# Performance work log

Hardware: AMD Instinct MI355X
Metric: run time of the kernel (lower is better)

## Reference

```python
import jax, jax.numpy as jnp
import numpy as np

V_A, V_HP = 256, 256
H_A, H_HP = 2048, 4096
DEPTH = 12


def lstm_cell(x, h, c, W_ih, W_hh, b_ih, b_hh):
    # PyTorch LSTM cell: gate order i, f, g, o along the 4H axis.
    gates = x @ W_ih.T + h @ W_hh.T + (b_ih + b_hh)
    i, f, g, o = jnp.split(gates, 4, axis=-1)
    c_new = jax.nn.sigmoid(f) * c + jax.nn.sigmoid(i) * jnp.tanh(g)
    h_new = jax.nn.sigmoid(o) * jnp.tanh(c_new)
    return h_new, c_new


def setup_inputs() -> dict:
    key = jax.random.key(0)
    ks = jax.random.split(key, 16)
    s = jnp.float32(0.02)
    f32 = jnp.float32
    return {
        "x_thought_vec_arch": jax.random.normal(ks[0], (1, 1, H_A), f32),
        "x_thought_vec_arch_hp": jax.random.normal(ks[1], (1, 1, H_HP), f32),
        # arch LSTM (input V_A, hidden H_A)
        "W_ih_a": jax.random.normal(ks[2], (4 * H_A, V_A), f32) * s,
        "W_hh_a": jax.random.normal(ks[3], (4 * H_A, H_A), f32) * s,
        "b_ih_a": jax.random.normal(ks[4], (4 * H_A,), f32) * s,
        "b_hh_a": jax.random.normal(ks[5], (4 * H_A,), f32) * s,
        # arch_out Linear (H_A -> V_A)
        "W_out_a": jax.random.normal(ks[6], (V_A, H_A), f32) * s,
        "b_out_a": jax.random.normal(ks[7], (V_A,), f32) * s,
        # hp_summarizer Linear (H_HP -> H_HP//2)
        "W_sum": jax.random.normal(ks[8], (H_HP // 2, H_HP), f32) * s,
        "b_sum": jax.random.normal(ks[9], (H_HP // 2,), f32) * s,
        # arch_hp LSTM (input V_A + V_HP, hidden H_HP)
        "W_ih_hp": jax.random.normal(ks[10], (4 * H_HP, V_A + V_HP), f32) * s,
        "W_hh_hp": jax.random.normal(ks[11], (4 * H_HP, H_HP), f32) * s,
        "b_ih_hp": jax.random.normal(ks[12], (4 * H_HP,), f32) * s,
        "b_hh_hp": jax.random.normal(ks[13], (4 * H_HP,), f32) * s,
        # arch_hp_out Linear (H_HP -> V_HP)
        "W_out_hp": jax.random.normal(ks[14], (V_HP, H_HP), f32) * s,
        "b_out_hp": jax.random.normal(ks[15], (V_HP,), f32) * s,
    }


def reference(x_thought_vec_arch, x_thought_vec_arch_hp,
              W_ih_a, W_hh_a, b_ih_a, b_hh_a, W_out_a, b_out_a,
              W_sum, b_sum, W_ih_hp, W_hh_hp, b_ih_hp, b_hh_hp,
              W_out_hp, b_out_hp):
    h_a, h_hp = x_thought_vec_arch, x_thought_vec_arch_hp  # thought vecs used as hidden states
    c_a = jnp.zeros_like(h_a)
    c_hp = jnp.zeros_like(h_hp)
    a = jnp.full((1, 1, V_A), 1.0 / V_A, jnp.float32)       # SOS soft one-hot
    a_hp = jnp.full((1, 1, V_HP), 1.0 / V_HP, jnp.float32)

    def step(carry, _):
        a, a_hp, h_a, c_a, h_hp, c_hp = carry
        # forward_arch: seq_len=1 so LSTM output == new hidden
        h_a, c_a = lstm_cell(a, h_a, c_a, W_ih_a, W_hh_a, b_ih_a, b_hh_a)
        a = jax.nn.softmax(h_a @ W_out_a.T + b_out_a, axis=-1)
        # forward_arch_hp (keeps the original's swapped hx=(c_hp, prev_h_hp)):
        h_sum = jax.nn.relu(h_hp @ W_sum.T + b_sum)
        prev_h_hp = jnp.concatenate([h_a, h_sum], axis=-1)   # used as CELL state
        inp = jnp.concatenate([a, a_hp], axis=-1)
        h_hp, c_hp = lstm_cell(inp, c_hp, prev_h_hp, W_ih_hp, W_hh_hp, b_ih_hp, b_hh_hp)
        a_hp = jax.nn.softmax(h_hp @ W_out_hp.T + b_out_hp, axis=-1)
        return (a, a_hp, h_a, c_a, h_hp, c_hp), (a, a_hp)

    _, (ys_a, ys_hp) = jax.lax.scan(step, (a, a_hp, h_a, c_a, h_hp, c_hp), None, length=DEPTH)
    # torch.cat(list_of_(1,1,V), dim=1) -> (1, DEPTH, V)
    arch = ys_a.reshape(DEPTH, V_A)[None]
    arch_hp = ys_hp.reshape(DEPTH, V_HP)[None]
    return arch, arch_hp
```

## Files before the change

### kernel.cpp

```cpp
#include <hip/hip_runtime.h>
#include <hip/hip_fp16.h>

#define H_A   2048
#define H_HP  4096
#define DEPTH 12

struct Half8 { __half2 a, b, c, d; };
struct Half4 { __half2 a, b; };

__device__ __forceinline__ float fsig_(float x) { return 1.0f / (1.0f + __expf(-x)); }
__device__ __forceinline__ float ftanh_(float x) {
    return 1.0f - 2.0f / (__expf(2.0f * x) + 1.0f);
}
__device__ __forceinline__ float dot4_(float4 a, float4 b) {
    return a.x * b.x + a.y * b.y + a.z * b.z + a.w * b.w;
}
__device__ __forceinline__ float dot8h_(Half8 w, float4 x0, float4 x1) {
    float2 wa = __half22float2(w.a), wb = __half22float2(w.b);
    float2 wc = __half22float2(w.c), wd = __half22float2(w.d);
    return wa.x * x0.x + wa.y * x0.y + wb.x * x0.z + wb.y * x0.w +
           wc.x * x1.x + wc.y * x1.y + wd.x * x1.z + wd.y * x1.w;
}
__device__ __forceinline__ Half4 cvt4_(float4 a) {
    Half4 h;
    h.a = __floats2half2_rn(a.x, a.y);
    h.b = __floats2half2_rn(a.z, a.w);
    return h;
}
__device__ __forceinline__ Half8 cvt8_(float4 a, float4 b) {
    Half8 h;
    h.a = __floats2half2_rn(a.x, a.y);
    h.b = __floats2half2_rn(a.z, a.w);
    h.c = __floats2half2_rn(b.x, b.y);
    h.d = __floats2half2_rn(b.z, b.w);
    return h;
}
__device__ __forceinline__ float waveReduceSum(float v) {
#pragma unroll
    for (int off = 32; off > 0; off >>= 1) v += __shfl_xor(v, off, 64);
    return v;
}
__device__ __forceinline__ void waveReduce4(float& a0, float& a1, float& a2, float& a3) {
#pragma unroll
    for (int off = 32; off > 0; off >>= 1) {
        a0 += __shfl_xor(a0, off, 64);
        a1 += __shfl_xor(a1, off, 64);
        a2 += __shfl_xor(a2, off, 64);
        a3 += __shfl_xor(a3, off, 64);
    }
}

struct Params {
    const float *x_a, *x_hp;
    const float *W_ih_a, *W_hh_a, *b_ih_a, *b_hh_a;
    const float *W_out_a, *b_out_a, *W_sum, *b_sum;
    const float *W_ih_hp, *W_hh_hp, *b_ih_hp, *b_hh_hp, *W_out_hp, *b_out_hp;
    __half *hW_ih_a, *hW_hh_a, *hW_sum, *hW_ih_hp, *hW_hh_hp, *hW_out_a, *hW_out_hp;
    float *gates_a, *h_sum, *gacc, *h_a, *c_a0, *c_a1, *h_hp, *c_hp;
    float *logits_a, *logits_hp, *a_vec, *out;
};

__global__ __launch_bounds__(256) void kA(Params p, int t)
{
    const int lane = threadIdx.x & 63;
    const int wave = (blockIdx.x << 2) | (threadIdx.x >> 6);

    if (wave < 8192) {
        const int r = wave;
        float acc;
        if (t == 0) {
            float4 wf = ((const float4*)(p.W_ih_a + (size_t)r * 256))[lane];
            ((Half4*)(p.hW_ih_a + (size_t)r * 256))[lane] = cvt4_(wf);
            acc = (wf.x + wf.y + wf.z + wf.w) * (1.0f / 256.0f);
            const float4* whf = (const float4*)(p.W_hh_a + (size_t)r * H_A);
            const float4* xh = (const float4*)p.x_a;
            Half4* dsth = (Half4*)(p.hW_hh_a + (size_t)r * H_A);
#pragma unroll
            for (int it = 0; it < 8; ++it) {
                int idx = it * 64 + lane;
                float4 w = whf[idx];
                dsth[idx] = cvt4_(w);
                acc += dot4_(w, xh[idx]);
            }
        } else {
            Half4 w = ((const Half4*)(p.hW_ih_a + (size_t)r * 256))[lane];
            float4 x = ((const float4*)p.a_vec)[lane];
            float2 w0 = __half22float2(w.a), w1 = __half22float2(w.b);
            acc = w0.x * x.x + w0.y * x.y + w1.x * x.z + w1.y * x.w;
            const Half8* wh = (const Half8*)(p.hW_hh_a + (size_t)r * H_A);
            const float4* xh = (const float4*)p.h_a;
#pragma unroll
            for (int it = 0; it < 4; ++it) {
                int idx = it * 64 + lane;
                acc += dot8h_(wh[idx], xh[2 * idx], xh[2 * idx + 1]);
            }
        }
        acc = waveReduceSum(acc);
        if (lane == 0) p.gates_a[r] = acc + p.b_ih_a[r] + p.b_hh_a[r];
    } else if (wave < 10240) {
        const int rr = wave - 8192;
        float acc = 0.0f;
        if (t == 0) {
            const float4* wf = (const float4*)(p.W_sum + (size_t)rr * H_HP);
            const float4* xx = (const float4*)p.x_hp;
            Half4* dsth = (Half4*)(p.hW_sum + (size_t)rr * H_HP);
#pragma unroll
            for (int it = 0; it < 16; ++it) {
                int idx = it * 64 + lane;
                float4 w = wf[idx];
                dsth[idx] = cvt4_(w);
                acc += dot4_(w, xx[idx]);
            }
        } else {
            const Half8* ww = (const Half8*)(p.hW_sum + (size_t)rr * H_HP);
            const float4* xx = (const float4*)p.h_hp;
#pragma unroll
            for (int it = 0; it < 8; ++it) {
                int idx = it * 64 + lane;
                acc += dot8h_(ww[idx], xx[2 * idx], xx[2 * idx + 1]);
            }
        }
        acc = waveReduceSum(acc);
        if (lane == 0) p.h_sum[rr] = fmaxf(acc + p.b_sum[rr], 0.0f);
    } else if (wave < 26624) {
        const int rg = wave - 10240;
        if (t == 0) {
            const float4* wf = (const float4*)(p.W_hh_hp + (size_t)rg * H_HP);
            Half4* dsth = (Half4*)(p.hW_hh_hp + (size_t)rg * H_HP);
#pragma unroll
            for (int it = 0; it < 16; ++it) {
                int idx = it * 64 + lane;
                dsth[idx] = cvt4_(wf[idx]);
            }
            if (lane == 0) p.gacc[rg] = p.b_ih_hp[rg] + p.b_hh_hp[rg];
        } else {
            const Half8* ww = (const Half8*)(p.hW_hh_hp + (size_t)rg * H_HP);
            const float4* xx = (const float4*)p.c_hp;
            float acc = 0.0f;
#pragma unroll
            for (int it = 0; it < 8; ++it) {
                int idx = it * 64 + lane;
                acc += dot8h_(ww[idx], xx[2 * idx], xx[2 * idx + 1]);
            }
            acc = waveReduceSum(acc);
            if (lane == 0) p.gacc[rg] = acc + p.b_ih_hp[rg] + p.b_hh_hp[rg];
        }
    } else {
        if (t == 0) return;
        const int ro = wave - 26624;
        float acc = 0.0f;
        const float4* xx = (const float4*)p.h_hp;
        if (t == 1) {
            const float4* wf = (const float4*)(p.W_out_hp + (size_t)ro * H_HP);
            Half4* dsth = (Half4*)(p.hW_out_hp + (size_t)ro * H_HP);
#pragma unroll
            for (int it = 0; it < 16; ++it) {
                int idx = it * 64 + lane;
                float4 w = wf[idx];
                dsth[idx] = cvt4_(w);
                acc += dot4_(w, xx[idx]);
            }
        } else {
            const Half8* ww = (const Half8*)(p.hW_out_hp + (size_t)ro * H_HP);
#pragma unroll
            for (int it = 0; it < 8; ++it) {
                int idx = it * 64 + lane;
                acc += dot8h_(ww[idx], xx[2 * idx], xx[2 * idx + 1]);
            }
        }
        acc = waveReduceSum(acc);
        if (lane == 0) p.logits_hp[ro] = acc + p.b_out_hp[ro];
    }
}

__global__ __launch_bounds__(256) void kB(Params p, int t)
{
    __shared__ float h_s[H_A];
    const int tid = threadIdx.x;
    const float* cin = (t & 1) ? p.c_a1 : p.c_a0;
    float* cout = (t & 1) ? p.c_a0 : p.c_a1;
#pragma unroll
    for (int k = 0; k < 8; ++k) {
        int e = tid + k * 256;
        float gi = p.gates_a[e], gf = p.gates_a[H_A + e];
        float gg = p.gates_a[2 * H_A + e], go = p.gates_a[3 * H_A + e];
        float ci = (t == 0) ? 0.0f : cin[e];
        float c = fsig_(gf) * ci + fsig_(gi) * ftanh_(gg);
        float h = fsig_(go) * ftanh_(c);
        h_s[e] = h;
        if (blockIdx.x == 0) { cout[e] = c; p.h_a[e] = h; }
    }
    __syncthreads();
    const int lane = tid & 63;
    const int r = (blockIdx.x << 2) | (tid >> 6);
    const float4* h4 = (const float4*)h_s;
    float acc = 0.0f;
    if (t == 0) {
        const float4* wf = (const float4*)(p.W_out_a + (size_t)r * H_A);
        Half4* dsth = (Half4*)(p.hW_out_a + (size_t)r * H_A);
#pragma unroll
        for (int it = 0; it < 8; ++it) {
            int idx = it * 64 + lane;
            float4 w = wf[idx];
            dsth[idx] = cvt4_(w);
            acc += dot4_(w, h4[idx]);
        }
    } else {
        const Half8* ww = (const Half8*)(p.hW_out_a + (size_t)r * H_A);
#pragma unroll
        for (int it = 0; it < 4; ++it) {
            int idx = it * 64 + lane;
            acc += dot8h_(ww[idx], h4[2 * idx], h4[2 * idx + 1]);
        }
    }
    acc = waveReduceSum(acc);
    if (lane == 0) p.logits_a[r] = acc + p.b_out_a[r];
}

__global__ __launch_bounds__(256) void kC(Params p, int t)
{
    __shared__ float p_all[512];
    __shared__ float red[8];
    const int tid = threadIdx.x, lane = tid & 63, wv = tid >> 6;
    float la = p.logits_a[tid];
    float lh = (t == 0) ? 0.0f : p.logits_hp[tid];
    float ma = la, mh = lh;
#pragma unroll
    for (int off = 32; off > 0; off >>= 1) {
        ma = fmaxf(ma, __shfl_xor(ma, off, 64));
        mh = fmaxf(mh, __shfl_xor(mh, off, 64));
    }
    if (lane == 0) { red[wv] = ma; red[4 + wv] = mh; }
    __syncthreads();
    ma = fmaxf(fmaxf(red[0], red[1]), fmaxf(red[2], red[3]));
    mh = fmaxf(fmaxf(red[4], red[5]), fmaxf(red[6], red[7]));
    __syncthreads();
    float ea = __expf(la - ma), eh = __expf(lh - mh);
    float sa = waveReduceSum(ea), sh = waveReduceSum(eh);
    if (lane == 0) { red[wv] = sa; red[4 + wv] = sh; }
    __syncthreads();
    sa = red[0] + red[1] + red[2] + red[3];
    sh = red[4] + red[5] + red[6] + red[7];
    float pa = ea / sa, ph = eh / sh;
    p_all[tid] = pa;
    p_all[256 + tid] = ph;
    if (blockIdx.x == 0) {
        p.a_vec[tid] = pa;
        p.out[(size_t)t * 256 + tid] = pa;
        if (t > 0) p.out[3072 + (size_t)(t - 1) * 256 + tid] = ph;
    }
    __syncthreads();
    float4 xa = ((const float4*)p_all)[2 * lane];
    float4 xb = ((const float4*)p_all)[2 * lane + 1];
    const int e = (blockIdx.x << 2) | wv;
    float s0, s1, s2, s3;
    if (t == 0) {
        auto rowdot_cvt = [&](int r) -> float {
            const float4* wf = (const float4*)(p.W_ih_hp + (size_t)r * 512);
            float4 u = wf[2 * lane], v = wf[2 * lane + 1];
            ((Half8*)(p.hW_ih_hp + (size_t)r * 512))[lane] = cvt8_(u, v);
            return dot4_(u, xa) + dot4_(v, xb);
        };
        s0 = rowdot_cvt(e);
        s1 = rowdot_cvt(4096 + e);
        s2 = rowdot_cvt(8192 + e);
        s3 = rowdot_cvt(12288 + e);
    } else {
        Half8 w0 = ((const Half8*)(p.hW_ih_hp + (size_t)e * 512))[lane];
        Half8 w1 = ((const Half8*)(p.hW_ih_hp + (size_t)(4096 + e) * 512))[lane];
        Half8 w2 = ((const Half8*)(p.hW_ih_hp + (size_t)(8192 + e) * 512))[lane];
        Half8 w3 = ((const Half8*)(p.hW_ih_hp + (size_t)(12288 + e) * 512))[lane];
        s0 = dot8h_(w0, xa, xb);
        s1 = dot8h_(w1, xa, xb);
        s2 = dot8h_(w2, xa, xb);
        s3 = dot8h_(w3, xa, xb);
    }
    waveReduce4(s0, s1, s2, s3);
    if (lane == 0) {
        float gi = s0 + p.gacc[e];
        float gf = s1 + p.gacc[4096 + e];
        float gg = s2 + p.gacc[8192 + e];
        float go = s3 + p.gacc[12288 + e];
        float prev = (e < H_A) ? p.h_a[e] : p.h_sum[e - H_A];
        float c = fsig_(gf) * prev + fsig_(gi) * ftanh_(gg);
        float h = fsig_(go) * ftanh_(c);
        p.c_hp[e] = c;
        p.h_hp[e] = h;
    }
}

__global__ __launch_bounds__(256) void kTail_gemv(Params p)
{
    const int lane = threadIdx.x & 63;
    const int r = (blockIdx.x << 2) | (threadIdx.x >> 6);
    const Half8* ww = (const Half8*)(p.hW_out_hp + (size_t)r * H_HP);
    const float4* xx = (const float4*)p.h_hp;
    float acc = 0.0f;
#pragma unroll
    for (int it = 0; it < 8; ++it) {
        int idx = it * 64 + lane;
        acc += dot8h_(ww[idx], xx[2 * idx], xx[2 * idx + 1]);
    }
    acc = waveReduceSum(acc);
    if (lane == 0) p.logits_hp[r] = acc + p.b_out_hp[r];
}

__global__ __launch_bounds__(256) void kTail_softmax(Params p)
{
    __shared__ float red[4];
    const int tid = threadIdx.x, lane = tid & 63, wv = tid >> 6;
    float v = p.logits_hp[tid];
    float m = v;
#pragma unroll
    for (int off = 32; off > 0; off >>= 1) m = fmaxf(m, __shfl_xor(m, off, 64));
    if (lane == 0) red[wv] = m;
    __syncthreads();
    m = fmaxf(fmaxf(red[0], red[1]), fmaxf(red[2], red[3]));
    __syncthreads();
    float e = __expf(v - m);
    float s = waveReduceSum(e);
    if (lane == 0) red[wv] = s;
    __syncthreads();
    s = red[0] + red[1] + red[2] + red[3];
    p.out[3072 + 11 * 256 + tid] = e / s;
}


extern "C" void kernel_launch(void* const* d_in, const int* in_sizes, int n_in,
                              void* d_out, int out_size, void* d_ws, size_t ws_size,
                              hipStream_t stream)
{
    Params p;
    p.x_a      = (const float*)d_in[0];
    p.x_hp     = (const float*)d_in[1];
    p.W_ih_a   = (const float*)d_in[2];
    p.W_hh_a   = (const float*)d_in[3];
    p.b_ih_a   = (const float*)d_in[4];
    p.b_hh_a   = (const float*)d_in[5];
    p.W_out_a  = (const float*)d_in[6];
    p.b_out_a  = (const float*)d_in[7];
    p.W_sum    = (const float*)d_in[8];
    p.b_sum    = (const float*)d_in[9];
    p.W_ih_hp  = (const float*)d_in[10];
    p.W_hh_hp  = (const float*)d_in[11];
    p.b_ih_hp  = (const float*)d_in[12];
    p.b_hh_hp  = (const float*)d_in[13];
    p.W_out_hp = (const float*)d_in[14];
    p.b_out_hp = (const float*)d_in[15];

    p.hW_ih_a   = (__half*)d_ws;
    p.hW_hh_a   = p.hW_ih_a   + 2097152;
    p.hW_sum    = p.hW_hh_a   + 16777216;
    p.hW_ih_hp  = p.hW_sum    + 8388608;
    p.hW_hh_hp  = p.hW_ih_hp  + 8388608;
    p.hW_out_a  = p.hW_hh_hp  + 67108864;
    p.hW_out_hp = p.hW_out_a  + 524288;
    float* ws = (float*)(p.hW_out_hp + 1048576);

    p.gates_a   = ws;
    p.h_sum     = ws + 8192;
    p.gacc      = ws + 10240;
    p.h_a       = ws + 26624;
    p.c_a0      = ws + 28672;
    p.c_a1      = ws + 30720;
    p.h_hp      = ws + 32768;
    p.c_hp      = ws + 36864;
    p.logits_a  = ws + 40960;
    p.logits_hp = ws + 41216;
    p.a_vec     = ws + 41472;
    p.out       = (float*)d_out;

    for (int t = 0; t < DEPTH; ++t) {
        kA<<<6720, 256, 0, stream>>>(p, t);
        kB<<<64, 256, 0, stream>>>(p, t);
        kC<<<1024, 256, 0, stream>>>(p, t);
    }
    kTail_gemv<<<64, 256, 0, stream>>>(p);
    kTail_softmax<<<1, 256, 0, stream>>>(p);
}
```

Baseline: 980.7 us.

## Use MFMA 16x16x32 f16 GEMV with tiled fp16 weight layout in kA

```diff
diff --git a/kernel.cpp b/kernel.cpp
--- a/kernel.cpp
+++ b/kernel.cpp
@@ -4,6 +4,10 @@
 #define H_A   2048
 #define H_HP  4096
 #define DEPTH 12
+#define KCOMB 2304
+
+typedef _Float16 f16x8 __attribute__((ext_vector_type(8)));
+typedef float    f32x4 __attribute__((ext_vector_type(4)));
 
 struct Half8 { __half2 a, b, c, d; };
 struct Half4 { __half2 a, b; };
@@ -35,6 +39,12 @@
     h.d = __floats2half2_rn(b.z, b.w);
     return h;
 }
+__device__ __forceinline__ f16x8 cvtf8_(float4 a, float4 b) {
+    f16x8 r;
+    r[0] = (_Float16)a.x; r[1] = (_Float16)a.y; r[2] = (_Float16)a.z; r[3] = (_Float16)a.w;
+    r[4] = (_Float16)b.x; r[5] = (_Float16)b.y; r[6] = (_Float16)b.z; r[7] = (_Float16)b.w;
+    return r;
+}
 __device__ __forceinline__ float waveReduceSum(float v) {
 #pragma unroll
     for (int off = 32; off > 0; off >>= 1) v += __shfl_xor(v, off, 64);
@@ -55,121 +65,94 @@
     const float *W_ih_a, *W_hh_a, *b_ih_a, *b_hh_a;
     const float *W_out_a, *b_out_a, *W_sum, *b_sum;
     const float *W_ih_hp, *W_hh_hp, *b_ih_hp, *b_hh_hp, *W_out_hp, *b_out_hp;
-    __half *hW_ih_a, *hW_hh_a, *hW_sum, *hW_ih_hp, *hW_hh_hp, *hW_out_a, *hW_out_hp;
+    __half *hW_a, *hW_sum, *hW_hh_hp, *hW_out_hp;
+    __half *hW_ih_hp, *hW_out_a;
+    __half *xa_h, *hhp_h, *chp_h;
     float *gates_a, *h_sum, *gacc, *h_a, *c_a0, *c_a1, *h_hp, *c_hp;
-    float *logits_a, *logits_hp, *a_vec, *out;
+    float *logits_a, *logits_hp, *out;
 };
 
 __global__ __launch_bounds__(256) void kA(Params p, int t)
 {
-    const int lane = threadIdx.x & 63;
-    const int wave = (blockIdx.x << 2) | (threadIdx.x >> 6);
-
-    if (wave < 8192) {
-        const int r = wave;
-        float acc;
-        if (t == 0) {
-            float4 wf = ((const float4*)(p.W_ih_a + (size_t)r * 256))[lane];
-            ((Half4*)(p.hW_ih_a + (size_t)r * 256))[lane] = cvt4_(wf);
-            acc = (wf.x + wf.y + wf.z + wf.w) * (1.0f / 256.0f);
-            const float4* whf = (const float4*)(p.W_hh_a + (size_t)r * H_A);
-            const float4* xh = (const float4*)p.x_a;
-            Half4* dsth = (Half4*)(p.hW_hh_a + (size_t)r * H_A);
-#pragma unroll
-            for (int it = 0; it < 8; ++it) {
-                int idx = it * 64 + lane;
-                float4 w = whf[idx];
-                dsth[idx] = cvt4_(w);
-                acc += dot4_(w, xh[idx]);
+    __shared__ float red[4][16];
+    const int tid = threadIdx.x, lane = tid & 63, wv = tid >> 6;
+    const int b = blockIdx.x;
+
+    int sec, rb, ntiles;
+    __half* Wf; const __half* xh;
+    if (b < 512)       { sec = 0; rb = b;        Wf = p.hW_a      + (size_t)rb * 16 * KCOMB; xh = p.xa_h;  ntiles = KCOMB / 32; }
+    else if (b < 640)  { sec = 1; rb = b - 512;  Wf = p.hW_sum    + (size_t)rb * 16 * H_HP;  xh = p.hhp_h; ntiles = H_HP / 32; }
+    else if (b < 1664) { sec = 2; rb = b - 640;  Wf = p.hW_hh_hp  + (size_t)rb * 16 * H_HP;  xh = p.chp_h; ntiles = H_HP / 32; }
+    else               { sec = 3; rb = b - 1664; Wf = p.hW_out_hp + (size_t)rb * 16 * H_HP;  xh = p.hhp_h; ntiles = H_HP / 32; }
+    const int ntl = ntiles >> 2;
+    const int kt0 = wv * ntl;
+
+    if (t > 0) {
+        f32x4 acc0 = {0.f, 0.f, 0.f, 0.f}, acc1 = {0.f, 0.f, 0.f, 0.f};
+        const int xoff = (lane >> 4) * 8;
+#pragma unroll 2
+        for (int i = 0; i < ntl; i += 2) {
+            const int kt = kt0 + i;
+            f16x8 a0 = *(const f16x8*)(Wf + (size_t)kt * 512 + lane * 8);
+            f16x8 b0 = *(const f16x8*)(xh + kt * 32 + xoff);
+            f16x8 a1 = *(const f16x8*)(Wf + (size_t)(kt + 1) * 512 + lane * 8);
+            f16x8 b1 = *(const f16x8*)(xh + (kt + 1) * 32 + xoff);
+            acc0 = __builtin_amdgcn_mfma_f32_16x16x32_f16(a0, b0, acc0, 0, 0, 0);
+            acc1 = __builtin_amdgcn_mfma_f32_16x16x32_f16(a1, b1, acc1, 0, 0, 0);
+        }
+        f32x4 acc = acc0 + acc1;
+        if ((lane & 15) == 0) {
+            const int r0 = (lane >> 4) * 4;
+            red[wv][r0]     = acc[0];
+            red[wv][r0 + 1] = acc[1];
+            red[wv][r0 + 2] = acc[2];
+            red[wv][r0 + 3] = acc[3];
+        }
+    } else {
+        float ppart = 0.0f;
+        const int row = rb * 16 + (lane & 15);
+        const int kc = (lane >> 4) * 8;
+        for (int i = 0; i < ntl; ++i) {
+            const int kt = kt0 + i;
+            const int k = kt * 32 + kc;
+            const float* src;
+            if (sec == 0)      src = (k < 256) ? p.W_ih_a + (size_t)row * 256 + k
+                                               : p.W_hh_a + (size_t)row * H_A + (k - 256);
+            else if (sec == 1) src = p.W_sum    + (size_t)row * H_HP + k;
+            else if (sec == 2) src = p.W_hh_hp  + (size_t)row * H_HP + k;
+            else               src = p.W_out_hp + (size_t)row * H_HP + k;
+            float4 u = ((const float4*)src)[0];
+            float4 v = ((const float4*)src)[1];
+            *(f16x8*)(Wf + (size_t)kt * 512 + lane * 8) = cvtf8_(u, v);
+            if (sec == 0) {
+                if (k < 256) {
+                    ppart += (u.x + u.y + u.z + u.w + v.x + v.y + v.z + v.w) * (1.0f / 256.0f);
+                } else {
+                    float4 xu = *(const float4*)(p.x_a + (k - 256));
+                    float4 xv = *(const float4*)(p.x_a + (k - 256) + 4);
+                    ppart += dot4_(u, xu) + dot4_(v, xv);
+                }
+            } else if (sec == 1) {
+                float4 xu = *(const float4*)(p.x_hp + k);
+                float4 xv = *(const float4*)(p.x_hp + k + 4);
+                ppart += dot4_(u, xu) + dot4_(v, xv);
             }
-        } else {
-            Half4 w = ((const Half4*)(p.hW_ih_a + (size_t)r * 256))[lane];
-            float4 x = ((const float4*)p.a_vec)[lane];
-            float2 w0 = __half22float2(w.a), w1 = __half22float2(w.b);
-            acc = w0.x * x.x + w0.y * x.y + w1.x * x.z + w1.y * x.w;
-            const Half8* wh = (const Half8*)(p.hW_hh_a + (size_t)r * H_A);
-            const float4* xh = (const float4*)p.h_a;
-#pragma unroll
-            for (int it = 0; it < 4; ++it) {
-                int idx = it * 64 + lane;
-                acc += dot8h_(wh[idx], xh[2 * idx], xh[2 * idx + 1]);
-            }
-        }
-        acc = waveReduceSum(acc);
-        if (lane == 0) p.gates_a[r] = acc + p.b_ih_a[r] + p.b_hh_a[r];
-    } else if (wave < 10240) {
-        const int rr = wave - 8192;
-        float acc = 0.0f;
-        if (t == 0) {
-            const float4* wf = (const float4*)(p.W_sum + (size_t)rr * H_HP);
-            const float4* xx = (const float4*)p.x_hp;
-            Half4* dsth = (Half4*)(p.hW_sum + (size_t)rr * H_HP);
-#pragma unroll
-            for (int it = 0; it < 16; ++it) {
-                int idx = it * 64 + lane;
-                float4 w = wf[idx];
-                dsth[idx] = cvt4_(w);
-                acc += dot4_(w, xx[idx]);
-            }
-        } else {
-            const Half8* ww = (const Half8*)(p.hW_sum + (size_t)rr * H_HP);
-            const float4* xx = (const float4*)p.h_hp;
-#pragma unroll
-            for (int it = 0; it < 8; ++it) {
-                int idx = it * 64 + lane;
-                acc += dot8h_(ww[idx], xx[2 * idx], xx[2 * idx + 1]);
-            }
-        }
-        acc = waveReduceSum(acc);
-        if (lane == 0) p.h_sum[rr] = fmaxf(acc + p.b_sum[rr], 0.0f);
-    } else if (wave < 26624) {
-        const int rg = wave - 10240;
-        if (t == 0) {
-            const float4* wf = (const float4*)(p.W_hh_hp + (size_t)rg * H_HP);
-            Half4* dsth = (Half4*)(p.hW_hh_hp + (size_t)rg * H_HP);
-#pragma unroll
-            for (int it = 0; it < 16; ++it) {
-                int idx = it * 64 + lane;
-                dsth[idx] = cvt4_(wf[idx]);
-            }
-            if (lane == 0) p.gacc[rg] = p.b_ih_hp[rg] + p.b_hh_hp[rg];
-        } else {
-            const Half8* ww = (const Half8*)(p.hW_hh_hp + (size_t)rg * H_HP);
-            const float4* xx = (const float4*)p.c_hp;
-            float acc = 0.0f;
-#pragma unroll
-            for (int it = 0; it < 8; ++it) {
-                int idx = it * 64 + lane;
-                acc += dot8h_(ww[idx], xx[2 * idx], xx[2 * idx + 1]);
-            }
-            acc = waveReduceSum(acc);
-            if (lane == 0) p.gacc[rg] = acc + p.b_ih_hp[rg] + p.b_hh_hp[rg];
-        }
-    } else {
-        if (t == 0) return;
-        const int ro = wave - 26624;
-        float acc = 0.0f;
-        const float4* xx = (const float4*)p.h_hp;
-        if (t == 1) {
-            const float4* wf = (const float4*)(p.W_out_hp + (size_t)ro * H_HP);
-            Half4* dsth = (Half4*)(p.hW_out_hp + (size_t)ro * H_HP);
-#pragma unroll
-            for (int it = 0; it < 16; ++it) {
-                int idx = it * 64 + lane;
-                float4 w = wf[idx];
-                dsth[idx] = cvt4_(w);
-                acc += dot4_(w, xx[idx]);
-            }
-        } else {
-            const Half8* ww = (const Half8*)(p.hW_out_hp + (size_t)ro * H_HP);
-#pragma unroll
-            for (int it = 0; it < 8; ++it) {
-                int idx = it * 64 + lane;
-                acc += dot8h_(ww[idx], xx[2 * idx], xx[2 * idx + 1]);
-            }
-        }
-        acc = waveReduceSum(acc);
-        if (lane == 0) p.logits_hp[ro] = acc + p.b_out_hp[ro];
+        }
+        ppart += __shfl_xor(ppart, 16, 64);
+        ppart += __shfl_xor(ppart, 32, 64);
+        if (lane < 16) red[wv][lane] = ppart;
+    }
+
+    __syncthreads();
+    if (tid < 16) {
+        const int g = rb * 16 + tid;
+        float s = 0.0f;
+        if (t > 0 || sec <= 1)
+            s = red[0][tid] + red[1][tid] + red[2][tid] + red[3][tid];
+        if (sec == 0)      p.gates_a[g] = s + p.b_ih_a[g] + p.b_hh_a[g];
+        else if (sec == 1) p.h_sum[g]   = fmaxf(s + p.b_sum[g], 0.0f);
+        else if (sec == 2) p.gacc[g]    = s + p.b_ih_hp[g] + p.b_hh_hp[g];
+        else if (t > 0)    p.logits_hp[g] = s + p.b_out_hp[g];
     }
 }
 
@@ -188,7 +171,11 @@
         float c = fsig_(gf) * ci + fsig_(gi) * ftanh_(gg);
         float h = fsig_(go) * ftanh_(c);
         h_s[e] = h;
-        if (blockIdx.x == 0) { cout[e] = c; p.h_a[e] = h; }
+        if (blockIdx.x == 0) {
+            cout[e] = c;
+            p.h_a[e] = h;
+            p.xa_h[256 + e] = __float2half(h);
+        }
     }
     __syncthreads();
     const int lane = tid & 63;
@@ -245,7 +232,7 @@
     p_all[tid] = pa;
     p_all[256 + tid] = ph;
     if (blockIdx.x == 0) {
-        p.a_vec[tid] = pa;
+        p.xa_h[tid] = __float2half(pa);
         p.out[(size_t)t * 256 + tid] = pa;
         if (t > 0) p.out[3072 + (size_t)(t - 1) * 256 + tid] = ph;
     }
@@ -286,23 +273,44 @@
         float h = fsig_(go) * ftanh_(c);
         p.c_hp[e] = c;
         p.h_hp[e] = h;
+        p.chp_h[e] = __float2half(c);
+        p.hhp_h[e] = __float2half(h);
     }
 }
 
 __global__ __launch_bounds__(256) void kTail_gemv(Params p)
 {
-    const int lane = threadIdx.x & 63;
-    const int r = (blockIdx.x << 2) | (threadIdx.x >> 6);
-    const Half8* ww = (const Half8*)(p.hW_out_hp + (size_t)r * H_HP);
-    const float4* xx = (const float4*)p.h_hp;
-    float acc = 0.0f;
-#pragma unroll
-    for (int it = 0; it < 8; ++it) {
-        int idx = it * 64 + lane;
-        acc += dot8h_(ww[idx], xx[2 * idx], xx[2 * idx + 1]);
-    }
-    acc = waveReduceSum(acc);
-    if (lane == 0) p.logits_hp[r] = acc + p.b_out_hp[r];
+    __shared__ float red[4][16];
+    const int tid = threadIdx.x, lane = tid & 63, wv = tid >> 6;
+    const int rb = blockIdx.x;
+    const __half* Wf = p.hW_out_hp + (size_t)rb * 16 * H_HP;
+    const __half* xh = p.hhp_h;
+    const int kt0 = wv * 32;
+    f32x4 acc0 = {0.f, 0.f, 0.f, 0.f}, acc1 = {0.f, 0.f, 0.f, 0.f};
+    const int xoff = (lane >> 4) * 8;
+#pragma unroll 2
+    for (int i = 0; i < 32; i += 2) {
+        const int kt = kt0 + i;
+        f16x8 a0 = *(const f16x8*)(Wf + (size_t)kt * 512 + lane * 8);
+        f16x8 b0 = *(const f16x8*)(xh + kt * 32 + xoff);
+        f16x8 a1 = *(const f16x8*)(Wf + (size_t)(kt + 1) * 512 + lane * 8);
+        f16x8 b1 = *(const f16x8*)(xh + (kt + 1) * 32 + xoff);
+        acc0 = __builtin_amdgcn_mfma_f32_16x16x32_f16(a0, b0, acc0, 0, 0, 0);
+        acc1 = __builtin_amdgcn_mfma_f32_16x16x32_f16(a1, b1, acc1, 0, 0, 0);
+    }
+    f32x4 acc = acc0 + acc1;
+    if ((lane & 15) == 0) {
+        const int r0 = (lane >> 4) * 4;
+        red[wv][r0]     = acc[0];
+        red[wv][r0 + 1] = acc[1];
+        red[wv][r0 + 2] = acc[2];
+        red[wv][r0 + 3] = acc[3];
+    }
+    __syncthreads();
+    if (tid < 16) {
+        const int g = rb * 16 + tid;
+        p.logits_hp[g] = red[0][tid] + red[1][tid] + red[2][tid] + red[3][tid] + p.b_out_hp[g];
+    }
 }
 
 __global__ __launch_bounds__(256) void kTail_softmax(Params p)
@@ -348,14 +356,16 @@
     p.W_out_hp = (const float*)d_in[14];
     p.b_out_hp = (const float*)d_in[15];
 
-    p.hW_ih_a   = (__half*)d_ws;
-    p.hW_hh_a   = p.hW_ih_a   + 2097152;
-    p.hW_sum    = p.hW_hh_a   + 16777216;
-    p.hW_ih_hp  = p.hW_sum    + 8388608;
-    p.hW_hh_hp  = p.hW_ih_hp  + 8388608;
-    p.hW_out_a  = p.hW_hh_hp  + 67108864;
-    p.hW_out_hp = p.hW_out_a  + 524288;
-    float* ws = (float*)(p.hW_out_hp + 1048576);
+    p.hW_a      = (__half*)d_ws;
+    p.hW_sum    = p.hW_a      + 18874368;
+    p.hW_hh_hp  = p.hW_sum    + 8388608;
+    p.hW_out_hp = p.hW_hh_hp  + 67108864;
+    p.hW_ih_hp  = p.hW_out_hp + 1048576;
+    p.hW_out_a  = p.hW_ih_hp  + 8388608;
+    p.xa_h      = p.hW_out_a  + 524288;
+    p.hhp_h     = p.xa_h      + 2304;
+    p.chp_h     = p.hhp_h     + 4096;
+    float* ws   = (float*)(p.chp_h + 4096);
 
     p.gates_a   = ws;
     p.h_sum     = ws + 8192;
@@ -367,14 +377,13 @@
     p.c_hp      = ws + 36864;
     p.logits_a  = ws + 40960;
     p.logits_hp = ws + 41216;
-    p.a_vec     = ws + 41472;
     p.out       = (float*)d_out;
 
     for (int t = 0; t < DEPTH; ++t) {
-        kA<<<6720, 256, 0, stream>>>(p, t);
+        kA<<<1680, 256, 0, stream>>>(p, t);
         kB<<<64, 256, 0, stream>>>(p, t);
         kC<<<1024, 256, 0, stream>>>(p, t);
     }
-    kTail_gemv<<<64, 256, 0, stream>>>(p);
+    kTail_gemv<<<16, 256, 0, stream>>>(p);
     kTail_softmax<<<1, 256, 0, stream>>>(p);
 }
```

Result: slower. 1.022 ms (+4.2%).
